# Kernel tuning notes

Hardware: AMD Instinct MI355X
Metric: run time of the kernel (lower is better)

The kernel has to match this reference:

```python
import jax, jax.numpy as jnp
import numpy as np


def log_g(x):
    # log of g(x) = relu(x)+0.5 for x>=0, sigmoid(x) for x<0 (continuous minGRU activation)
    return jnp.where(x >= 0, jnp.log(jax.nn.relu(x) + 0.5), -jax.nn.softplus(-x))


def parallel_scan_log(log_coeffs, log_values):
    # log_coeffs: [B,T,H], log_values: [B,T+1,H]
    a_star = jnp.pad(jnp.cumsum(log_coeffs, axis=1), ((0, 0), (1, 0), (0, 0)))  # [B,T+1,H]
    log_h = a_star + jax.lax.cumlogsumexp(log_values - a_star, axis=1)
    return jnp.exp(log_h)  # [B,T+1,H]


def setup_inputs() -> dict:
    key = jax.random.key(0)
    B, T, D, H = 8, 4096, 1024, 1024
    k1, k2, k3, k4, k5, k6 = jax.random.split(key, 6)
    scale = 1.0 / np.sqrt(D)
    return {
        "x": jax.random.normal(k1, (B, T, D), dtype=jnp.float32),
        "h_0": jax.random.uniform(k2, (B, 1, H), dtype=jnp.float32),
        "W_z": jax.random.uniform(k3, (H, D), minval=-scale, maxval=scale, dtype=jnp.float32),
        "b_z": jax.random.uniform(k4, (H,), minval=-scale, maxval=scale, dtype=jnp.float32),
        "W_h": jax.random.uniform(k5, (H, D), minval=-scale, maxval=scale, dtype=jnp.float32),
        "b_h": jax.random.uniform(k6, (H,), minval=-scale, maxval=scale, dtype=jnp.float32),
    }


def reference(x, h_0, W_z, b_z, W_h, b_h):
    # k = linear_z(x)
    k = jnp.einsum('btd,hd->bth', x, W_z) + b_z                 # [B,T,H]
    log_z = -jax.nn.softplus(-k)                                # log sigmoid(k)
    log_coeffs = -jax.nn.softplus(k)                            # log (1 - sigmoid(k))
    log_h_0 = log_g(h_0)                                        # [B,1,H]
    log_tilde_h = log_g(jnp.einsum('btd,hd->bth', x, W_h) + b_h)  # [B,T,H]
    log_values = jnp.concatenate([log_h_0, log_z + log_tilde_h], axis=1)  # [B,T+1,H]
    h = parallel_scan_log(log_coeffs, log_values)               # [B,T+1,H]
    return h
```

## Files before the change

kernel.cpp:

```cpp
#include <hip/hip_runtime.h>
#include <stdint.h>

#define B_ 8
#define T_ 4096
#define D_ 1024
#define H_ 1024
#define M_ (B_*T_)
#define K_ D_
#define N_ H_
#define TC 64
#define NC (T_/TC)
#define NKT (K_/64)

typedef short short8 __attribute__((ext_vector_type(8)));
typedef float f32x4 __attribute__((ext_vector_type(4)));
typedef unsigned short ushort8v __attribute__((ext_vector_type(8)));

__device__ __forceinline__ float bf2f(unsigned short u) {
    union { unsigned int i; float f; } x; x.i = ((unsigned int)u) << 16; return x.f;
}
__device__ __forceinline__ unsigned short f2bf(float f) {
    union { float f; unsigned int i; } x; x.f = f;
    unsigned int u = x.i;
    unsigned int r = u + 0x7fffu + ((u >> 16) & 1u);
    return (unsigned short)(r >> 16);
}
__device__ __forceinline__ void gld_lds16(const unsigned short* g, unsigned short* l) {
    __builtin_amdgcn_global_load_lds(
        (const __attribute__((address_space(1))) void*)(const void*)g,
        (__attribute__((address_space(3))) void*)(void*)l, 16, 0, 0);
}
__device__ __forceinline__ float gfun(float x) {
    return x >= 0.f ? x + 0.5f : 1.f / (1.f + __expf(-x));
}

__global__ void cvt_kernel(const float* __restrict__ src, unsigned short* __restrict__ dst, int n4) {
    int i = blockIdx.x * blockDim.x + threadIdx.x;
    const int stride = gridDim.x * blockDim.x;
    for (; i < n4; i += stride) {
        float4 v = ((const float4*)src)[i];
        ushort4 o;
        o.x = f2bf(v.x); o.y = f2bf(v.y); o.z = f2bf(v.z); o.w = f2bf(v.w);
        ((ushort4*)dst)[i] = o;
    }
}

#define SB() __builtin_amdgcn_sched_barrier(0)
#define BAR() do { SB(); __builtin_amdgcn_s_barrier(); SB(); } while (0)

__global__ __launch_bounds__(512, 2) void gemm_kernel(
    const unsigned short* __restrict__ Xb,
    const unsigned short* __restrict__ Wzb,
    const unsigned short* __restrict__ Whb,
    const float* __restrict__ bz, const float* __restrict__ bh,
    unsigned short* __restrict__ KzOut, unsigned short* __restrict__ KhOut)
{
    __shared__ __align__(16) unsigned short ldsA[2][256 * 64];
    __shared__ __align__(16) unsigned short ldsB[2][256 * 64];

    const int bm = blockIdx.x;
    const int bn = blockIdx.y;
    const int mat = blockIdx.z;
    const unsigned short* Wb = mat ? Whb : Wzb;
    const float* bias = mat ? bh : bz;
    unsigned short* Out = mat ? KhOut : KzOut;

    const int tid = threadIdx.x;
    const int w = tid >> 6, lane = tid & 63;
    const int wm = w >> 2, wn = w & 3;

    const int srow = lane >> 3;
    const int schunk = ((lane & 7) ^ srow) << 3;
    const unsigned short* gA = Xb + (size_t)(bm * 256 + srow) * K_ + schunk;
    const unsigned short* gB = Wb + (size_t)(bn * 256 + srow) * K_ + schunk;

#define STAGE_A(s, kt, h) do { \
    gld_lds16(gA + (size_t)((h)*128 + 0*64 + w*8) * K_ + (kt)*64, &ldsA[s][((h)*128 + 0*64 + w*8) * 64]); \
    gld_lds16(gA + (size_t)((h)*128 + 1*64 + w*8) * K_ + (kt)*64, &ldsA[s][((h)*128 + 1*64 + w*8) * 64]); \
  } while (0)
#define STAGE_B(s, kt, h) do { \
    gld_lds16(gB + (size_t)((h)*128 + 0*64 + w*8) * K_ + (kt)*64, &ldsB[s][((h)*128 + 0*64 + w*8) * 64]); \
    gld_lds16(gB + (size_t)((h)*128 + 1*64 + w*8) * K_ + (kt)*64, &ldsB[s][((h)*128 + 1*64 + w*8) * 64]); \
  } while (0)

    const int lrow = lane & 15;
    const int q = lane >> 4;
    const int sw0 = (q ^ (lane & 7)) << 3;

#define LDA(s, fm, kh) (*(const short8*)&ldsA[s][(wm*128 + (fm)*16 + lrow) * 64 + (sw0 ^ ((kh)*32))])
#define LDB(s, fn, kh) (*(const short8*)&ldsB[s][(wn*64  + (fn)*16 + lrow) * 64 + (sw0 ^ ((kh)*32))])

#define RD_A4(s, fmb) do { \
    _Pragma("unroll") for (int f = 0; f < 4; ++f) { Ar[f][0] = LDA(s, (fmb)+f, 0); Ar[f][1] = LDA(s, (fmb)+f, 1); } \
  } while (0)
#define RD_B2(s, fnb) do { \
    _Pragma("unroll") for (int g = 0; g < 2; ++g) { Br[(fnb)+g][0] = LDB(s, (fnb)+g, 0); Br[(fnb)+g][1] = LDB(s, (fnb)+g, 1); } \
  } while (0)

#define QUAD(mb, nb) do { \
    __builtin_amdgcn_s_setprio(1); \
    _Pragma("unroll") for (int f = 0; f < 4; ++f) { \
      _Pragma("unroll") for (int g = 0; g < 2; ++g) { \
        acc[(mb)+f][(nb)+g] = __builtin_amdgcn_mfma_f32_16x16x32_bf16(Ar[f][0], Br[(nb)+g][0], acc[(mb)+f][(nb)+g], 0, 0, 0); \
        acc[(mb)+f][(nb)+g] = __builtin_amdgcn_mfma_f32_16x16x32_bf16(Ar[f][1], Br[(nb)+g][1], acc[(mb)+f][(nb)+g], 0, 0, 0); \
      } \
    } \
    __builtin_amdgcn_s_setprio(0); \
  } while (0)

    f32x4 acc[8][4];
#pragma unroll
    for (int i = 0; i < 8; ++i)
#pragma unroll
        for (int j = 0; j < 4; ++j) acc[i][j] = (f32x4){0.f, 0.f, 0.f, 0.f};
    short8 Ar[4][2], Br[4][2];

    STAGE_B(0, 0, 0); STAGE_B(0, 0, 1);
    STAGE_A(0, 0, 0); STAGE_A(0, 0, 1);
    STAGE_B(1, 1, 0); STAGE_B(1, 1, 1);
    SB();
    asm volatile("s_waitcnt vmcnt(4)" ::: "memory");
    BAR();

#pragma unroll 1
    for (int i = 0; i < 8; ++i) {
        const int kt1 = 2 * i + 1;
        const int kt2 = 2 * i + 2;
        const int kt3 = 2 * i + 3;
        const bool st = (i < 7);

        RD_A4(0, 0); RD_B2(0, 0);
        STAGE_A(1, kt1, 0);
        BAR();
        QUAD(0, 0);
        BAR();
        RD_B2(0, 2);
        STAGE_A(1, kt1, 1);
        BAR();
        QUAD(0, 2);
        BAR();
        RD_A4(0, 4);
        if (st) STAGE_B(0, kt2, 0);
        BAR();
        QUAD(4, 0);
        BAR();
        if (st) {
            STAGE_B(0, kt2, 1);
            SB();
            asm volatile("s_waitcnt vmcnt(4)" ::: "memory");
        } else {
            asm volatile("s_waitcnt vmcnt(0)" ::: "memory");
        }
        BAR();
        QUAD(4, 2);
        BAR();
        RD_A4(1, 0); RD_B2(1, 0);
        if (st) STAGE_A(0, kt2, 0);
        BAR();
        QUAD(0, 0);
        BAR();
        RD_B2(1, 2);
        if (st) STAGE_A(0, kt2, 1);
        BAR();
        QUAD(0, 2);
        BAR();
        RD_A4(1, 4);
        if (st) STAGE_B(1, kt3, 0);
        BAR();
        QUAD(4, 0);
        BAR();
        if (st) {
            STAGE_B(1, kt3, 1);
            SB();
            asm volatile("s_waitcnt vmcnt(4)" ::: "memory");
        }
        BAR();
        QUAD(4, 2);
        BAR();
    }

#pragma unroll
    for (int fn = 0; fn < 4; ++fn) {
        const int n = bn * 256 + wn * 64 + fn * 16 + lrow;
        const float bb = bias[n];
#pragma unroll
        for (int fm = 0; fm < 8; ++fm) {
            const int mq = bm * 64 + wm * 32 + fm * 4 + q;
            ushort4 o;
            o.x = f2bf(acc[fm][fn][0] + bb);
            o.y = f2bf(acc[fm][fn][1] + bb);
            o.z = f2bf(acc[fm][fn][2] + bb);
            o.w = f2bf(acc[fm][fn][3] + bb);
            *(ushort4*)(Out + ((size_t)mq * N_ + n) * 4) = o;
        }
    }
}


__global__ __launch_bounds__(256) void scanA_kernel(const unsigned short* __restrict__ Kz,
                                                    const unsigned short* __restrict__ Kh,
                                                    float* __restrict__ Fc, float* __restrict__ Vc)
{
    const int c = blockIdx.x, b = blockIdx.y;
    const int hb = threadIdx.x * 4;
    float F[4] = {1.f, 1.f, 1.f, 1.f}, V[4] = {0.f, 0.f, 0.f, 0.f};
    size_t base = ((size_t)(b * 1024 + c * (TC / 4)) * N_ + hb) * 4;
    for (int q = 0; q < TC / 4; q++) {
        ushort8v z0 = *(const ushort8v*)(Kz + base);
        ushort8v z1 = *(const ushort8v*)(Kz + base + 8);
        ushort8v h0v = *(const ushort8v*)(Kh + base);
        ushort8v h1v = *(const ushort8v*)(Kh + base + 8);
        base += (size_t)N_ * 4;
#pragma unroll
        for (int r = 0; r < 4; r++) {
            float kzf[4] = {bf2f(z0[r]), bf2f(z0[4 + r]), bf2f(z1[r]), bf2f(z1[4 + r])};
            float khf[4] = {bf2f(h0v[r]), bf2f(h0v[4 + r]), bf2f(h1v[r]), bf2f(h1v[4 + r])};
#pragma unroll
            for (int j = 0; j < 4; j++) {
                float f = 1.f / (1.f + __expf(kzf[j]));
                float v = (1.f - f) * gfun(khf[j]);
                V[j] = f * V[j] + v;
                F[j] *= f;
            }
        }
    }
    size_t o = ((size_t)(b * NC + c)) * H_ + hb;
    *(float4*)(Fc + o) = make_float4(F[0], F[1], F[2], F[3]);
    *(float4*)(Vc + o) = make_float4(V[0], V[1], V[2], V[3]);
}

__global__ __launch_bounds__(256) void scanB_kernel(const float* __restrict__ h0,
                                                    const float* __restrict__ Fc,
                                                    const float* __restrict__ Vc,
                                                    float* __restrict__ Carry,
                                                    float* __restrict__ Out)
{
    const int b = blockIdx.x;
    const int h = threadIdx.x * 4;
    float cy[4];
#pragma unroll
    for (int j = 0; j < 4; j++) cy[j] = gfun(h0[(size_t)b * H_ + h + j]);
    *(float4*)(Out + (size_t)b * (T_ + 1) * H_ + h) = make_float4(cy[0], cy[1], cy[2], cy[3]);
    for (int c = 0; c < NC; c++) {
        size_t o = ((size_t)(b * NC + c)) * H_ + h;
        *(float4*)(Carry + o) = make_float4(cy[0], cy[1], cy[2], cy[3]);
        float4 F4 = *(const float4*)(Fc + o);
        float4 V4 = *(const float4*)(Vc + o);
        cy[0] = F4.x * cy[0] + V4.x;
        cy[1] = F4.y * cy[1] + V4.y;
        cy[2] = F4.z * cy[2] + V4.z;
        cy[3] = F4.w * cy[3] + V4.w;
    }
}

__global__ __launch_bounds__(256) void scanC_kernel(const unsigned short* __restrict__ Kz,
                                                    const unsigned short* __restrict__ Kh,
                                                    const float* __restrict__ Carry,
                                                    float* __restrict__ Out)
{
    const int c = blockIdx.x, b = blockIdx.y;
    const int hb = threadIdx.x * 4;
    float cy[4];
    {
        float4 c4 = *(const float4*)(Carry + ((size_t)(b * NC + c)) * H_ + hb);
        cy[0] = c4.x; cy[1] = c4.y; cy[2] = c4.z; cy[3] = c4.w;
    }
    size_t base = ((size_t)(b * 1024 + c * (TC / 4)) * N_ + hb) * 4;
    size_t ob = ((size_t)(b * (T_ + 1) + c * TC + 1)) * H_ + hb;
    for (int q = 0; q < TC / 4; q++) {
        ushort8v z0 = *(const ushort8v*)(Kz + base);
        ushort8v z1 = *(const ushort8v*)(Kz + base + 8);
        ushort8v h0v = *(const ushort8v*)(Kh + base);
        ushort8v h1v = *(const ushort8v*)(Kh + base + 8);
        base += (size_t)N_ * 4;
#pragma unroll
        for (int r = 0; r < 4; r++) {
            float kzf[4] = {bf2f(z0[r]), bf2f(z0[4 + r]), bf2f(z1[r]), bf2f(z1[4 + r])};
            float khf[4] = {bf2f(h0v[r]), bf2f(h0v[4 + r]), bf2f(h1v[r]), bf2f(h1v[4 + r])};
#pragma unroll
            for (int j = 0; j < 4; j++) {
                float f = 1.f / (1.f + __expf(kzf[j]));
                float v = (1.f - f) * gfun(khf[j]);
                cy[j] = f * cy[j] + v;
            }
            *(float4*)(Out + ob) = make_float4(cy[0], cy[1], cy[2], cy[3]);
            ob += H_;
        }
    }
}

extern "C" void kernel_launch(void* const* d_in, const int* in_sizes, int n_in,
                              void* d_out, int out_size, void* d_ws, size_t ws_size,
                              hipStream_t stream)
{
    const float* x  = (const float*)d_in[0];
    const float* h0 = (const float*)d_in[1];
    const float* Wz = (const float*)d_in[2];
    const float* bz = (const float*)d_in[3];
    const float* Wh = (const float*)d_in[4];
    const float* bh = (const float*)d_in[5];
    float* out = (float*)d_out;

    char* ws = (char*)d_ws;
    unsigned short* xb  = (unsigned short*)ws; ws += (size_t)M_ * K_ * 2;
    unsigned short* wzb = (unsigned short*)ws; ws += (size_t)N_ * K_ * 2;
    unsigned short* whb = (unsigned short*)ws; ws += (size_t)N_ * K_ * 2;
    unsigned short* kz  = (unsigned short*)ws; ws += (size_t)M_ * N_ * 2;
    unsigned short* kh  = (unsigned short*)ws; ws += (size_t)M_ * N_ * 2;
    float* Fc    = (float*)ws; ws += (size_t)B_ * NC * H_ * 4;
    float* Vc    = (float*)ws; ws += (size_t)B_ * NC * H_ * 4;
    float* Carry = (float*)ws; ws += (size_t)B_ * NC * H_ * 4;

    cvt_kernel<<<2048, 256, 0, stream>>>(x, xb, M_ * K_ / 4);
    cvt_kernel<<<256, 256, 0, stream>>>(Wz, wzb, N_ * K_ / 4);
    cvt_kernel<<<256, 256, 0, stream>>>(Wh, whb, N_ * K_ / 4);

    dim3 gg(M_ / 256, N_ / 256, 2);
    gemm_kernel<<<gg, 512, 0, stream>>>(xb, wzb, whb, bz, bh, kz, kh);

    scanA_kernel<<<dim3(NC, B_), 256, 0, stream>>>(kz, kh, Fc, Vc);
    scanB_kernel<<<B_, 256, 0, stream>>>(h0, Fc, Vc, Carry, out);
    scanC_kernel<<<dim3(NC, B_), 256, 0, stream>>>(kz, kh, Carry, out);
}
```

Before: 466.9 us.

## Make GEMM persistent over four M-tiles, halve scan chunk, widen and prefetch scanB

The GEMM grid now launches a quarter as many blocks along M. Each block loops over four consecutive 256-row tiles and keeps the staging pipeline running across tile boundaries, with bias loaded once. The scan chunk size drops from 64 to 32 timesteps, which doubles the parallelism in scanA/scanC but doubles the serial length of scanB. To offset that, scanB is split across H into 4 blocks per batch and prefetches the next chunk's F/V values. The two weight conversions are merged into one launch, which cuts launch overhead and lets the GEMM's load pipeline span tiles. The risk is a smaller GEMM grid (256 blocks), which may underfill the GPU's compute units.

```diff
diff --git a/kernel.cpp b/kernel.cpp
--- a/kernel.cpp
+++ b/kernel.cpp
@@ -8,9 +8,8 @@
 #define M_ (B_*T_)
 #define K_ D_
 #define N_ H_
-#define TC 64
+#define TC 32
 #define NC (T_/TC)
-#define NKT (K_/64)
 
 typedef short short8 __attribute__((ext_vector_type(8)));
 typedef float f32x4 __attribute__((ext_vector_type(4)));
@@ -45,6 +44,20 @@
     }
 }
 
+__global__ void cvtw_kernel(const float* __restrict__ Wz, const float* __restrict__ Wh,
+                            unsigned short* __restrict__ wzb, unsigned short* __restrict__ whb, int n4) {
+    const float* src = blockIdx.y ? Wh : Wz;
+    unsigned short* dst = blockIdx.y ? whb : wzb;
+    int i = blockIdx.x * blockDim.x + threadIdx.x;
+    const int stride = gridDim.x * blockDim.x;
+    for (; i < n4; i += stride) {
+        float4 v = ((const float4*)src)[i];
+        ushort4 o;
+        o.x = f2bf(v.x); o.y = f2bf(v.y); o.z = f2bf(v.z); o.w = f2bf(v.w);
+        ((ushort4*)dst)[i] = o;
+    }
+}
+
 #define SB() __builtin_amdgcn_sched_barrier(0)
 #define BAR() do { SB(); __builtin_amdgcn_s_barrier(); SB(); } while (0)
 
@@ -58,7 +71,7 @@
     __shared__ __align__(16) unsigned short ldsA[2][256 * 64];
     __shared__ __align__(16) unsigned short ldsB[2][256 * 64];
 
-    const int bm = blockIdx.x;
+    const int bx = blockIdx.x;
     const int bn = blockIdx.y;
     const int mat = blockIdx.z;
     const unsigned short* Wb = mat ? Whb : Wzb;
@@ -71,16 +84,20 @@
 
     const int srow = lane >> 3;
     const int schunk = ((lane & 7) ^ srow) << 3;
-    const unsigned short* gA = Xb + (size_t)(bm * 256 + srow) * K_ + schunk;
+    const unsigned short* gA = Xb + (size_t)(bx * 1024 + srow) * K_ + schunk;
     const unsigned short* gB = Wb + (size_t)(bn * 256 + srow) * K_ + schunk;
 
-#define STAGE_A(s, kt, h) do { \
-    gld_lds16(gA + (size_t)((h)*128 + 0*64 + w*8) * K_ + (kt)*64, &ldsA[s][((h)*128 + 0*64 + w*8) * 64]); \
-    gld_lds16(gA + (size_t)((h)*128 + 1*64 + w*8) * K_ + (kt)*64, &ldsA[s][((h)*128 + 1*64 + w*8) * 64]); \
-  } while (0)
-#define STAGE_B(s, kt, h) do { \
-    gld_lds16(gB + (size_t)((h)*128 + 0*64 + w*8) * K_ + (kt)*64, &ldsB[s][((h)*128 + 0*64 + w*8) * 64]); \
-    gld_lds16(gB + (size_t)((h)*128 + 1*64 + w*8) * K_ + (kt)*64, &ldsB[s][((h)*128 + 1*64 + w*8) * 64]); \
+#define STAGE_A(s, g, h) do { \
+    gld_lds16(gA + (size_t)(((g) >> 4) * 256 + (h)*128 + w*8) * K_ + ((g)&15) * 64, \
+              &ldsA[s][((h)*128 + w*8) * 64]); \
+    gld_lds16(gA + (size_t)(((g) >> 4) * 256 + (h)*128 + 64 + w*8) * K_ + ((g)&15) * 64, \
+              &ldsA[s][((h)*128 + 64 + w*8) * 64]); \
+  } while (0)
+#define STAGE_B(s, g, h) do { \
+    gld_lds16(gB + (size_t)((h)*128 + w*8) * K_ + ((g)&15) * 64, \
+              &ldsB[s][((h)*128 + w*8) * 64]); \
+    gld_lds16(gB + (size_t)((h)*128 + 64 + w*8) * K_ + ((g)&15) * 64, \
+              &ldsB[s][((h)*128 + 64 + w*8) * 64]); \
   } while (0)
 
     const int lrow = lane & 15;
@@ -94,26 +111,26 @@
     _Pragma("unroll") for (int f = 0; f < 4; ++f) { Ar[f][0] = LDA(s, (fmb)+f, 0); Ar[f][1] = LDA(s, (fmb)+f, 1); } \
   } while (0)
 #define RD_B2(s, fnb) do { \
-    _Pragma("unroll") for (int g = 0; g < 2; ++g) { Br[(fnb)+g][0] = LDB(s, (fnb)+g, 0); Br[(fnb)+g][1] = LDB(s, (fnb)+g, 1); } \
+    _Pragma("unroll") for (int g2_ = 0; g2_ < 2; ++g2_) { Br[(fnb)+g2_][0] = LDB(s, (fnb)+g2_, 0); Br[(fnb)+g2_][1] = LDB(s, (fnb)+g2_, 1); } \
   } while (0)
 
 #define QUAD(mb, nb) do { \
     __builtin_amdgcn_s_setprio(1); \
     _Pragma("unroll") for (int f = 0; f < 4; ++f) { \
-      _Pragma("unroll") for (int g = 0; g < 2; ++g) { \
-        acc[(mb)+f][(nb)+g] = __builtin_amdgcn_mfma_f32_16x16x32_bf16(Ar[f][0], Br[(nb)+g][0], acc[(mb)+f][(nb)+g], 0, 0, 0); \
-        acc[(mb)+f][(nb)+g] = __builtin_amdgcn_mfma_f32_16x16x32_bf16(Ar[f][1], Br[(nb)+g][1], acc[(mb)+f][(nb)+g], 0, 0, 0); \
+      _Pragma("unroll") for (int g2_ = 0; g2_ < 2; ++g2_) { \
+        acc[(mb)+f][(nb)+g2_] = __builtin_amdgcn_mfma_f32_16x16x32_bf16(Ar[f][0], Br[(nb)+g2_][0], acc[(mb)+f][(nb)+g2_], 0, 0, 0); \
+        acc[(mb)+f][(nb)+g2_] = __builtin_amdgcn_mfma_f32_16x16x32_bf16(Ar[f][1], Br[(nb)+g2_][1], acc[(mb)+f][(nb)+g2_], 0, 0, 0); \
       } \
     } \
     __builtin_amdgcn_s_setprio(0); \
   } while (0)
 
     f32x4 acc[8][4];
-#pragma unroll
-    for (int i = 0; i < 8; ++i)
-#pragma unroll
-        for (int j = 0; j < 4; ++j) acc[i][j] = (f32x4){0.f, 0.f, 0.f, 0.f};
     short8 Ar[4][2], Br[4][2];
+
+    float bb[4];
+#pragma unroll
+    for (int fn = 0; fn < 4; ++fn) bb[fn] = bias[bn * 256 + wn * 64 + fn * 16 + lrow];
 
     STAGE_B(0, 0, 0); STAGE_B(0, 0, 1);
     STAGE_A(0, 0, 0); STAGE_A(0, 0, 1);
@@ -123,75 +140,82 @@
     BAR();
 
 #pragma unroll 1
-    for (int i = 0; i < 8; ++i) {
-        const int kt1 = 2 * i + 1;
-        const int kt2 = 2 * i + 2;
-        const int kt3 = 2 * i + 3;
-        const bool st = (i < 7);
-
-        RD_A4(0, 0); RD_B2(0, 0);
-        STAGE_A(1, kt1, 0);
-        BAR();
-        QUAD(0, 0);
-        BAR();
-        RD_B2(0, 2);
-        STAGE_A(1, kt1, 1);
-        BAR();
-        QUAD(0, 2);
-        BAR();
-        RD_A4(0, 4);
-        if (st) STAGE_B(0, kt2, 0);
-        BAR();
-        QUAD(4, 0);
-        BAR();
-        if (st) {
-            STAGE_B(0, kt2, 1);
-            SB();
-            asm volatile("s_waitcnt vmcnt(4)" ::: "memory");
-        } else {
-            asm volatile("s_waitcnt vmcnt(0)" ::: "memory");
-        }
-        BAR();
-        QUAD(4, 2);
-        BAR();
-        RD_A4(1, 0); RD_B2(1, 0);
-        if (st) STAGE_A(0, kt2, 0);
-        BAR();
-        QUAD(0, 0);
-        BAR();
-        RD_B2(1, 2);
-        if (st) STAGE_A(0, kt2, 1);
-        BAR();
-        QUAD(0, 2);
-        BAR();
-        RD_A4(1, 4);
-        if (st) STAGE_B(1, kt3, 0);
-        BAR();
-        QUAD(4, 0);
-        BAR();
-        if (st) {
-            STAGE_B(1, kt3, 1);
-            SB();
-            asm volatile("s_waitcnt vmcnt(4)" ::: "memory");
-        }
-        BAR();
-        QUAD(4, 2);
-        BAR();
-    }
-
-#pragma unroll
-    for (int fn = 0; fn < 4; ++fn) {
-        const int n = bn * 256 + wn * 64 + fn * 16 + lrow;
-        const float bb = bias[n];
-#pragma unroll
-        for (int fm = 0; fm < 8; ++fm) {
-            const int mq = bm * 64 + wm * 32 + fm * 4 + q;
-            ushort4 o;
-            o.x = f2bf(acc[fm][fn][0] + bb);
-            o.y = f2bf(acc[fm][fn][1] + bb);
-            o.z = f2bf(acc[fm][fn][2] + bb);
-            o.w = f2bf(acc[fm][fn][3] + bb);
-            *(ushort4*)(Out + ((size_t)mq * N_ + n) * 4) = o;
+    for (int t = 0; t < 4; ++t) {
+#pragma unroll
+        for (int i = 0; i < 8; ++i)
+#pragma unroll
+            for (int j = 0; j < 4; ++j) acc[i][j] = (f32x4){0.f, 0.f, 0.f, 0.f};
+
+#pragma unroll 1
+        for (int i = 0; i < 8; ++i) {
+            const int g1 = t * 16 + 2 * i + 1;
+            const int g2 = g1 + 1;
+            const int g3 = g1 + 2;
+            const bool st = (g2 < 64);
+
+            RD_A4(0, 0); RD_B2(0, 0);
+            STAGE_A(1, g1, 0);
+            BAR();
+            QUAD(0, 0);
+            BAR();
+            RD_B2(0, 2);
+            STAGE_A(1, g1, 1);
+            BAR();
+            QUAD(0, 2);
+            BAR();
+            RD_A4(0, 4);
+            if (st) STAGE_B(0, g2, 0);
+            BAR();
+            QUAD(4, 0);
+            BAR();
+            if (st) {
+                STAGE_B(0, g2, 1);
+                SB();
+                asm volatile("s_waitcnt vmcnt(4)" ::: "memory");
+            } else {
+                asm volatile("s_waitcnt vmcnt(0)" ::: "memory");
+            }
+            BAR();
+            QUAD(4, 2);
+            BAR();
+            RD_A4(1, 0); RD_B2(1, 0);
+            if (st) STAGE_A(0, g2, 0);
+            BAR();
+            QUAD(0, 0);
+            BAR();
+            RD_B2(1, 2);
+            if (st) STAGE_A(0, g2, 1);
+            BAR();
+            QUAD(0, 2);
+            BAR();
+            RD_A4(1, 4);
+            if (st) STAGE_B(1, g3, 0);
+            BAR();
+            QUAD(4, 0);
+            BAR();
+            if (st) {
+                STAGE_B(1, g3, 1);
+                SB();
+                asm volatile("s_waitcnt vmcnt(4)" ::: "memory");
+            }
+            BAR();
+            QUAD(4, 2);
+            BAR();
+        }
+
+#pragma unroll
+        for (int fn = 0; fn < 4; ++fn) {
+            const int n = bn * 256 + wn * 64 + fn * 16 + lrow;
+#pragma unroll
+            for (int fm = 0; fm < 8; ++fm) {
+                const int mq = (bx * 4 + t) * 64 + wm * 32 + fm * 4 + q;
+                ushort4 o;
+                o.x = f2bf(acc[fm][fn][0] + bb[fn]);
+                o.y = f2bf(acc[fm][fn][1] + bb[fn]);
+                o.z = f2bf(acc[fm][fn][2] + bb[fn]);
+                o.w = f2bf(acc[fm][fn][3] + bb[fn]);
+                *(ushort4*)(Out + ((size_t)mq * N_ + n) * 4) = o;
+            }
         }
     }
 }
@@ -204,8 +228,8 @@
     const int c = blockIdx.x, b = blockIdx.y;
     const int hb = threadIdx.x * 4;
     float F[4] = {1.f, 1.f, 1.f, 1.f}, V[4] = {0.f, 0.f, 0.f, 0.f};
-    size_t base = ((size_t)(b * 1024 + c * (TC / 4)) * N_ + hb) * 4;
-    for (int q = 0; q < TC / 4; q++) {
+    size_t base = ((size_t)(b * (T_ / 4) + c * (TC / 4)) * N_ + hb) * 4;
+    for (int qq = 0; qq < TC / 4; qq++) {
         ushort8v z0 = *(const ushort8v*)(Kz + base);
         ushort8v z1 = *(const ushort8v*)(Kz + base + 8);
         ushort8v h0v = *(const ushort8v*)(Kh + base);
@@ -229,27 +253,34 @@
     *(float4*)(Vc + o) = make_float4(V[0], V[1], V[2], V[3]);
 }
 
-__global__ __launch_bounds__(256) void scanB_kernel(const float* __restrict__ h0,
-                                                    const float* __restrict__ Fc,
-                                                    const float* __restrict__ Vc,
-                                                    float* __restrict__ Carry,
-                                                    float* __restrict__ Out)
+__global__ __launch_bounds__(64) void scanB_kernel(const float* __restrict__ h0,
+                                                   const float* __restrict__ Fc,
+                                                   const float* __restrict__ Vc,
+                                                   float* __restrict__ Carry,
+                                                   float* __restrict__ Out)
 {
     const int b = blockIdx.x;
-    const int h = threadIdx.x * 4;
+    const int h = blockIdx.y * 256 + threadIdx.x * 4;
     float cy[4];
 #pragma unroll
     for (int j = 0; j < 4; j++) cy[j] = gfun(h0[(size_t)b * H_ + h + j]);
     *(float4*)(Out + (size_t)b * (T_ + 1) * H_ + h) = make_float4(cy[0], cy[1], cy[2], cy[3]);
+    size_t o = ((size_t)(b * NC)) * H_ + h;
+    float4 F4 = *(const float4*)(Fc + o);
+    float4 V4 = *(const float4*)(Vc + o);
     for (int c = 0; c < NC; c++) {
-        size_t o = ((size_t)(b * NC + c)) * H_ + h;
+        const size_t on = o + H_;
+        float4 nF, nV;
+        if (c + 1 < NC) {
+            nF = *(const float4*)(Fc + on);
+            nV = *(const float4*)(Vc + on);
+        }
         *(float4*)(Carry + o) = make_float4(cy[0], cy[1], cy[2], cy[3]);
-        float4 F4 = *(const float4*)(Fc + o);
-        float4 V4 = *(const float4*)(Vc + o);
         cy[0] = F4.x * cy[0] + V4.x;
         cy[1] = F4.y * cy[1] + V4.y;
         cy[2] = F4.z * cy[2] + V4.z;
         cy[3] = F4.w * cy[3] + V4.w;
+        F4 = nF; V4 = nV; o = on;
     }
 }
 
@@ -265,9 +296,9 @@
         float4 c4 = *(const float4*)(Carry + ((size_t)(b * NC + c)) * H_ + hb);
         cy[0] = c4.x; cy[1] = c4.y; cy[2] = c4.z; cy[3] = c4.w;
     }
-    size_t base = ((size_t)(b * 1024 + c * (TC / 4)) * N_ + hb) * 4;
+    size_t base = ((size_t)(b * (T_ / 4) + c * (TC / 4)) * N_ + hb) * 4;
     size_t ob = ((size_t)(b * (T_ + 1) + c * TC + 1)) * H_ + hb;
-    for (int q = 0; q < TC / 4; q++) {
+    for (int qq = 0; qq < TC / 4; qq++) {
         ushort8v z0 = *(const ushort8v*)(Kz + base);
         ushort8v z1 = *(const ushort8v*)(Kz + base + 8);
         ushort8v h0v = *(const ushort8v*)(Kh + base);
@@ -312,13 +343,12 @@
     float* Carry = (float*)ws; ws += (size_t)B_ * NC * H_ * 4;
 
     cvt_kernel<<<2048, 256, 0, stream>>>(x, xb, M_ * K_ / 4);
-    cvt_kernel<<<256, 256, 0, stream>>>(Wz, wzb, N_ * K_ / 4);
-    cvt_kernel<<<256, 256, 0, stream>>>(Wh, whb, N_ * K_ / 4);
-
-    dim3 gg(M_ / 256, N_ / 256, 2);
+    cvtw_kernel<<<dim3(128, 2), 256, 0, stream>>>(Wz, Wh, wzb, whb, N_ * K_ / 4);
+
+    dim3 gg(M_ / 1024, N_ / 256, 2);
     gemm_kernel<<<gg, 512, 0, stream>>>(xb, wzb, whb, bz, bh, kz, kh);
 
     scanA_kernel<<<dim3(NC, B_), 256, 0, stream>>>(kz, kh, Fc, Vc);
-    scanB_kernel<<<B_, 256, 0, stream>>>(h0, Fc, Vc, Carry, out);
+    scanB_kernel<<<dim3(B_, H_ / 256), 64, 0, stream>>>(h0, Fc, Vc, Carry, out);
     scanC_kernel<<<dim3(NC, B_), 256, 0, stream>>>(kz, kh, Carry, out);
 }
```

Measured after the change: 459.7 us. No clear change (-1.5%).
